# Performance work log

Hardware: AMD Instinct MI355X
Metric: run time of the kernel (lower is better)

## Reference

```python
import jax, jax.numpy as jnp
import numpy as np

NUM_STATES = 32768
NUM_LABELS = 64
BATCH = 512


def setup_inputs() -> dict:
    key = jax.random.key(0)
    k1, k2, k3, k4 = jax.random.split(key, 4)
    f = jax.random.normal(k1, (BATCH, NUM_LABELS), dtype=jnp.float32)
    # legal_state: binary indicator matrix [num_states, num_labels]
    S = jax.random.randint(k2, (NUM_STATES, NUM_LABELS), 0, 2).astype(jnp.float32)
    y = jax.random.uniform(k3, (BATCH, NUM_LABELS), dtype=jnp.float32)
    mask = jax.random.randint(k4, (BATCH, NUM_LABELS), 0, 2).astype(jnp.float32)
    return {"f": f, "S": S, "y": y, "mask": mask}


def reference(f, S, y, mask):
    # potential[s, b] = sum_i S[s, i] * f[b, i]
    potential = jnp.einsum('si,bi->sb', S, f)
    # stable softmax over the state axis (replaces exp/max/sum in original)
    P = jax.nn.softmax(potential, axis=0)  # [num_states, batch]
    # pMargin[b, i] = sum_{s: S[s,i]>0} P[s, b]  ->  indicator-matrix GEMM
    pMargin = jnp.einsum('sb,si->bi', P, S)  # [batch, num_labels]
    # per-column BCE (torch BCELoss clamps log at -100), masked, mean over batch
    logp = jnp.clip(jnp.log(pMargin), -100.0, None)
    log1mp = jnp.clip(jnp.log(1.0 - pMargin), -100.0, None)
    bce = -(y * logp + (1.0 - y) * log1mp) * mask  # [batch, num_labels]
    loss = jnp.sum(jnp.mean(bce, axis=0))  # sum over columns of per-column means
    return loss, pMargin
```

## Files before the change

kernel.cpp:

```cpp
#include <hip/hip_runtime.h>
#include <hip/hip_bf16.h>
#include <math.h>

#define N_STATES 32768
#define N_LABELS 64
#define N_BATCH  512

#define WS_Z    64
#define WS_M    576
#define WS_U    1088
#define SB_BYTE  262144u
#define STB_BYTE (SB_BYTE + 4194304u)

typedef __attribute__((ext_vector_type(8))) short          bfrag;
typedef __attribute__((ext_vector_type(4))) float          f32x4;
typedef __attribute__((ext_vector_type(8))) unsigned short u16x8;

static __device__ __forceinline__ unsigned short f2bf(float x) {
    __hip_bfloat16 h = __float2bfloat16(x);
    return *reinterpret_cast<unsigned short*>(&h);
}
static __device__ __forceinline__ float bf2f(unsigned short u) {
    __hip_bfloat16 h;
    *reinterpret_cast<unsigned short*>(&h) = u;
    return __bfloat162float(h);
}

typedef __attribute__((address_space(1))) const unsigned char g_u8;
typedef __attribute__((address_space(3))) unsigned char       l_u8;
static __device__ __forceinline__ void dma16(const void* g, void* l) {
    __builtin_amdgcn_global_load_lds((g_u8*)g, (l_u8*)l, 16, 0, 0);
}

__global__ __launch_bounds__(256) void prep_kernel(
    const float* __restrict__ f, const float* __restrict__ S,
    float* __restrict__ ws, float* __restrict__ out) {
    const int tb = blockIdx.x;
    const int t  = threadIdx.x;

    if (tb == 512) {
        if (t == 0) out[0] = 0.f;
        for (int b = t; b < N_BATCH; b += 256) {
            ws[WS_Z + b] = 0.f;
            const float* fr = f + b * N_LABELS;
            float m = 0.f;
            #pragma unroll
            for (int i = 0; i < N_LABELS; i++) m += fmaxf(fr[i], 0.f);
            ws[WS_M + b] = m;
        }
        return;
    }

    if (t < 64) ws[WS_U + tb * 64 + t] = 0.f;

    __shared__ alignas(16) unsigned short Sl[64 * 72];

    unsigned short* SbW = (unsigned short*)((char*)ws + SB_BYTE);
    unsigned short* StW = (unsigned short*)((char*)ws + STB_BYTE);

    const int r = t >> 2;
    const int q = t & 3;
    const int m = r & 7;

    const float4* p4 = reinterpret_cast<const float4*>(
        S + ((size_t)(tb * 64 + r)) * N_LABELS + q * 16);
    float4 v0 = p4[0], v1 = p4[1], v2 = p4[2], v3 = p4[3];
    float vf[16] = {v0.x,v0.y,v0.z,v0.w, v1.x,v1.y,v1.z,v1.w,
                    v2.x,v2.y,v2.z,v2.w, v3.x,v3.y,v3.z,v3.w};
    u16x8 lo8, hi8;
    #pragma unroll
    for (int j = 0; j < 8; j++) { lo8[j] = f2bf(vf[j]); hi8[j] = f2bf(vf[8 + j]); }

    *(u16x8*)&Sl[r * 72 + q * 16]     = lo8;
    *(u16x8*)&Sl[r * 72 + q * 16 + 8] = hi8;

    {
        unsigned short* dst = SbW + (size_t)tb * 4096 + r * 64 + (((2 * q) ^ (m & 6)) * 8);
        if (m & 1) { *(u16x8*)dst = hi8; *(u16x8*)(dst + 8) = lo8; }
        else       { *(u16x8*)dst = lo8; *(u16x8*)(dst + 8) = hi8; }
    }
    __syncthreads();

    const int i  = r;
    const int mi = i & 7;
    u16x8 tlo, thi;
    #pragma unroll
    for (int j = 0; j < 8; j++) {
        tlo[j] = Sl[(16 * q + j)     * 72 + i];
        thi[j] = Sl[(16 * q + 8 + j) * 72 + i];
    }
    {
        unsigned short* dst = StW + (size_t)tb * 4096 + i * 64 + (((2 * q) ^ (mi & 6)) * 8);
        if (mi & 1) { *(u16x8*)dst = thi; *(u16x8*)(dst + 8) = tlo; }
        else        { *(u16x8*)dst = tlo; *(u16x8*)(dst + 8) = thi; }
    }
}

__global__ __launch_bounds__(256, 2) void fused_kernel(
    const float* __restrict__ f, float* __restrict__ ws) {
    __shared__ alignas(16) unsigned short Sb2[2][4096];
    __shared__ alignas(16) unsigned short St2[2][4096];
    __shared__ alignas(16) unsigned short Et[64 * 72];

    float* Z = ws + WS_Z;
    const float* M = ws + WS_M;
    float* U = ws + WS_U;
    const char* SbG = (const char*)ws + SB_BYTE;
    const char* StG = (const char*)ws + STB_BYTE;

    const int t     = threadIdx.x;
    const int lane  = t & 63;
    const int w     = t >> 6;
    const int x     = lane & 15;
    const int quad  = lane >> 4;
    const int mm    = x & 7;
    const int btile = blockIdx.x >> 6;
    const int chunk = blockIdx.x & 63;
    const int tile0 = chunk * 8;

    bfrag fh[4][2], fl[4][2];
    #pragma unroll
    for (int nt = 0; nt < 4; nt++) {
        const float4* fp = reinterpret_cast<const float4*>(
            f + ((size_t)(btile * 64 + nt * 16 + x)) * N_LABELS);
        #pragma unroll
        for (int kh = 0; kh < 2; kh++) {
            float4 a = fp[kh * 8 + quad * 2];
            float4 b = fp[kh * 8 + quad * 2 + 1];
            float vv[8] = {a.x,a.y,a.z,a.w, b.x,b.y,b.z,b.w};
            #pragma unroll
            for (int j = 0; j < 8; j++) {
                unsigned short h = f2bf(vv[j]);
                fh[nt][kh][j] = (short)h;
                fl[nt][kh][j] = (short)f2bf(vv[j] - bf2f(h));
            }
        }
    }
    float Mv[4];
    #pragma unroll
    for (int nt = 0; nt < 4; nt++) Mv[nt] = M[btile * 64 + nt * 16 + x];

    f32x4 Uacc[4];
    #pragma unroll
    for (int nt = 0; nt < 4; nt++) Uacc[nt] = (f32x4){0.f, 0.f, 0.f, 0.f};
    float zacc[4] = {0.f, 0.f, 0.f, 0.f};

    auto stage = [&](int tile, int buf) {
        size_t gb = (size_t)tile * 8192 + (size_t)w * 2048 + (size_t)lane * 16;
        int lo = w * 2048;
        dma16(SbG + gb,        (char*)&Sb2[buf][0] + lo);
        dma16(SbG + gb + 1024, (char*)&Sb2[buf][0] + lo + 1024);
        dma16(StG + gb,        (char*)&St2[buf][0] + lo);
        dma16(StG + gb + 1024, (char*)&St2[buf][0] + lo + 1024);
    };

    stage(tile0 + 0, 0);
    stage(tile0 + 1, 1);
    asm volatile("s_waitcnt vmcnt(4)" ::: "memory");
    asm volatile("s_barrier" ::: "memory");

    #pragma unroll
    for (int st = 0; st < 8; st++) {
        const int cur = st & 1;
        const unsigned short* Sb = &Sb2[cur][0];
        const unsigned short* St = &St2[cur][0];

        bfrag a0 = *(const bfrag*)(Sb + (16 * w + x) * 64 + ((quad ^ mm) * 8));
        bfrag a1 = *(const bfrag*)(Sb + (16 * w + x) * 64 + (((quad + 4) ^ mm) * 8));
        #pragma unroll
        for (int nt = 0; nt < 4; nt++) {
            f32x4 acc = (f32x4){0.f, 0.f, 0.f, 0.f};
            acc = __builtin_amdgcn_mfma_f32_16x16x32_bf16(a0, fh[nt][0], acc, 0, 0, 0);
            acc = __builtin_amdgcn_mfma_f32_16x16x32_bf16(a1, fh[nt][1], acc, 0, 0, 0);
            acc = __builtin_amdgcn_mfma_f32_16x16x32_bf16(a0, fl[nt][0], acc, 0, 0, 0);
            acc = __builtin_amdgcn_mfma_f32_16x16x32_bf16(a1, fl[nt][1], acc, 0, 0, 0);
            float e0 = __expf(acc[0] - Mv[nt]);
            float e1 = __expf(acc[1] - Mv[nt]);
            float e2 = __expf(acc[2] - Mv[nt]);
            float e3 = __expf(acc[3] - Mv[nt]);
            zacc[nt] += (e0 + e1) + (e2 + e3);
            ushort4 ev;
            ev.x = f2bf(e0); ev.y = f2bf(e1); ev.z = f2bf(e2); ev.w = f2bf(e3);
            *(ushort4*)&Et[(nt * 16 + x) * 72 + 16 * w + quad * 4] = ev;
        }
        asm volatile("s_waitcnt lgkmcnt(0)" ::: "memory");
        asm volatile("s_barrier" ::: "memory");

        bfrag c0 = *(const bfrag*)(St + (16 * w + x) * 64 + ((quad ^ mm) * 8));
        bfrag c1 = *(const bfrag*)(St + (16 * w + x) * 64 + (((quad + 4) ^ mm) * 8));
        #pragma unroll
        for (int nt = 0; nt < 4; nt++) {
            bfrag e0 = *(const bfrag*)(Et + (nt * 16 + x) * 72 + quad * 8);
            bfrag e1 = *(const bfrag*)(Et + (nt * 16 + x) * 72 + 32 + quad * 8);
            Uacc[nt] = __builtin_amdgcn_mfma_f32_16x16x32_bf16(c0, e0, Uacc[nt], 0, 0, 0);
            Uacc[nt] = __builtin_amdgcn_mfma_f32_16x16x32_bf16(c1, e1, Uacc[nt], 0, 0, 0);
        }

        if (st < 6) {
            asm volatile("s_barrier" ::: "memory");
            stage(tile0 + st + 2, cur);
            asm volatile("s_waitcnt vmcnt(4)" ::: "memory");
            asm volatile("s_barrier" ::: "memory");
        } else if (st == 6) {
            asm volatile("s_waitcnt vmcnt(0)" ::: "memory");
            asm volatile("s_barrier" ::: "memory");
        }
    }

    #pragma unroll
    for (int nt = 0; nt < 4; nt++) {
        #pragma unroll
        for (int r = 0; r < 4; r++) {
            int i = 16 * w + quad * 4 + r;
            int b = btile * 64 + nt * 16 + x;
            atomicAdd(&U[i * N_BATCH + b], Uacc[nt][r]);
        }
    }
    #pragma unroll
    for (int nt = 0; nt < 4; nt++) {
        float v = zacc[nt];
        v += __shfl_down(v, 32, 64);
        v += __shfl_down(v, 16, 64);
        if (quad == 0) atomicAdd(&Z[btile * 64 + nt * 16 + x], v);
    }
}

__global__ void finalize_kernel(const float* __restrict__ ws,
                                const float* __restrict__ y,
                                const float* __restrict__ mask,
                                float* __restrict__ out) {
    const float* Z = ws + WS_Z;
    const float* U = ws + WS_U;

    int idx = blockIdx.x * 256 + threadIdx.x;
    int b = idx >> 6;
    int i = idx & 63;

    float p = U[i * N_BATCH + b] / Z[b];
    p = fminf(fmaxf(p, 0.f), 1.f);
    out[1 + idx] = p;

    float lp  = fmaxf(logf(p), -100.f);
    float l1p = fmaxf(logf(1.f - p), -100.f);
    float yy = y[idx];
    float bce = -(yy * lp + (1.f - yy) * l1p) * mask[idx] * (1.f / (float)N_BATCH);

    float v = bce;
    #pragma unroll
    for (int off = 32; off > 0; off >>= 1) v += __shfl_down(v, off, 64);
    __shared__ float wsum[4];
    if ((threadIdx.x & 63) == 0) wsum[threadIdx.x >> 6] = v;
    __syncthreads();
    if (threadIdx.x == 0)
        atomicAdd(&out[0], wsum[0] + wsum[1] + wsum[2] + wsum[3]);
}

extern "C" void kernel_launch(void* const* d_in, const int* in_sizes, int n_in,
                              void* d_out, int out_size, void* d_ws, size_t ws_size,
                              hipStream_t stream) {
    const float* f    = (const float*)d_in[0];
    const float* S    = (const float*)d_in[1];
    const float* y    = (const float*)d_in[2];
    const float* mask = (const float*)d_in[3];
    float* out = (float*)d_out;
    float* ws  = (float*)d_ws;

    prep_kernel<<<513, 256, 0, stream>>>(f, S, ws, out);
    fused_kernel<<<512, 256, 0, stream>>>(f, ws);
    finalize_kernel<<<128, 256, 0, stream>>>(ws, y, mask, out);
}
```

Before: 102.3 us.

## Replace global atomics with per-chunk partial buffers reduced in finalize

Each fused block now writes its U and Z partial sums for its state chunk to a dedicated slot in the workspace with plain stores, instead of issuing atomicAdds into shared U/Z arrays. The finalize kernel then sums the 64 chunk partials for each (label, batch) before computing probabilities and BCE. Zeroing moves out of prep, and the output scalar is cleared in the fused kernel. The aim is to remove atomic contention, at the cost of writing and rereading about 8 MB of partials plus a serial 64-term loop in finalize.

```diff
diff --git a/kernel.cpp b/kernel.cpp
--- a/kernel.cpp
+++ b/kernel.cpp
@@ -6,11 +6,11 @@
 #define N_LABELS 64
 #define N_BATCH  512
 
-#define WS_Z    64
-#define WS_M    576
-#define WS_U    1088
-#define SB_BYTE  262144u
-#define STB_BYTE (SB_BYTE + 4194304u)
+#define WS_M_F   0
+#define ZP_F     1024
+#define UP_F     65536
+#define SB_BYTE  8650752u
+#define STB_BYTE 12845056u
 
 typedef __attribute__((ext_vector_type(8))) short          bfrag;
 typedef __attribute__((ext_vector_type(4))) float          f32x4;
@@ -34,24 +34,20 @@
 
 __global__ __launch_bounds__(256) void prep_kernel(
     const float* __restrict__ f, const float* __restrict__ S,
-    float* __restrict__ ws, float* __restrict__ out) {
+    float* __restrict__ ws) {
     const int tb = blockIdx.x;
     const int t  = threadIdx.x;
 
     if (tb == 512) {
-        if (t == 0) out[0] = 0.f;
         for (int b = t; b < N_BATCH; b += 256) {
-            ws[WS_Z + b] = 0.f;
             const float* fr = f + b * N_LABELS;
             float m = 0.f;
             #pragma unroll
             for (int i = 0; i < N_LABELS; i++) m += fmaxf(fr[i], 0.f);
-            ws[WS_M + b] = m;
+            ws[WS_M_F + b] = m;
         }
         return;
     }
-
-    if (t < 64) ws[WS_U + tb * 64 + t] = 0.f;
 
     __shared__ alignas(16) unsigned short Sl[64 * 72];
 
@@ -97,14 +93,13 @@
 }
 
 __global__ __launch_bounds__(256, 2) void fused_kernel(
-    const float* __restrict__ f, float* __restrict__ ws) {
+    const float* __restrict__ f, float* __restrict__ ws,
+    float* __restrict__ out) {
     __shared__ alignas(16) unsigned short Sb2[2][4096];
     __shared__ alignas(16) unsigned short St2[2][4096];
     __shared__ alignas(16) unsigned short Et[64 * 72];
 
-    float* Z = ws + WS_Z;
-    const float* M = ws + WS_M;
-    float* U = ws + WS_U;
+    const float* M = ws + WS_M_F;
     const char* SbG = (const char*)ws + SB_BYTE;
     const char* StG = (const char*)ws + STB_BYTE;
 
@@ -207,37 +202,49 @@
         }
     }
 
+    float* Up = ws + UP_F;
     #pragma unroll
     for (int nt = 0; nt < 4; nt++) {
         #pragma unroll
         for (int r = 0; r < 4; r++) {
             int i = 16 * w + quad * 4 + r;
-            int b = btile * 64 + nt * 16 + x;
-            atomicAdd(&U[i * N_BATCH + b], Uacc[nt][r]);
-        }
-    }
+            Up[((btile * 64 + i) * 64 + chunk) * 64 + nt * 16 + x] = Uacc[nt][r];
+        }
+    }
+
+    __syncthreads();
+    float* zsh = (float*)Et;
     #pragma unroll
     for (int nt = 0; nt < 4; nt++) {
         float v = zacc[nt];
         v += __shfl_down(v, 32, 64);
         v += __shfl_down(v, 16, 64);
-        if (quad == 0) atomicAdd(&Z[btile * 64 + nt * 16 + x], v);
-    }
-}
-
-__global__ void finalize_kernel(const float* __restrict__ ws,
-                                const float* __restrict__ y,
-                                const float* __restrict__ mask,
-                                float* __restrict__ out) {
-    const float* Z = ws + WS_Z;
-    const float* U = ws + WS_U;
-
-    int idx = blockIdx.x * 256 + threadIdx.x;
-    int b = idx >> 6;
-    int i = idx & 63;
-
-    float p = U[i * N_BATCH + b] / Z[b];
-    p = fminf(fmaxf(p, 0.f), 1.f);
+        if (quad == 0) zsh[w * 64 + nt * 16 + x] = v;
+    }
+    __syncthreads();
+    if (t < 64) {
+        float z = zsh[t] + zsh[64 + t] + zsh[128 + t] + zsh[192 + t];
+        (ws + ZP_F)[(btile * 64 + chunk) * 64 + t] = z;
+    }
+    if (blockIdx.x == 0 && t == 0) out[0] = 0.f;
+}
+
+__global__ __launch_bounds__(256) void finalize_kernel(
+    const float* __restrict__ ws, const float* __restrict__ y,
+    const float* __restrict__ mask, float* __restrict__ out) {
+    const int i     = blockIdx.x >> 1;
+    const int b     = ((blockIdx.x & 1) << 8) + threadIdx.x;
+    const int btile = b >> 6;
+    const int bl    = b & 63;
+
+    const float* zp = ws + ZP_F + (btile * 64) * 64 + bl;
+    const float* up = ws + UP_F + ((btile * 64 + i) * 64) * 64 + bl;
+    float z = 0.f, u = 0.f;
+    #pragma unroll 8
+    for (int c = 0; c < 64; c++) { z += zp[c * 64]; u += up[c * 64]; }
+
+    float p = fminf(fmaxf(u / z, 0.f), 1.f);
+    const int idx = b * 64 + i;
     out[1 + idx] = p;
 
     float lp  = fmaxf(logf(p), -100.f);
@@ -265,7 +272,7 @@
     float* out = (float*)d_out;
     float* ws  = (float*)d_ws;
 
-    prep_kernel<<<513, 256, 0, stream>>>(f, S, ws, out);
-    fused_kernel<<<512, 256, 0, stream>>>(f, ws);
+    prep_kernel<<<513, 256, 0, stream>>>(f, S, ws);
+    fused_kernel<<<512, 256, 0, stream>>>(f, ws, out);
     finalize_kernel<<<128, 256, 0, stream>>>(ws, y, mask, out);
 }
```

After: 96.55 us. 1.06x faster.
